# Optimization experiments

Measured on AMD Instinct MI355X. Metric: run time of the kernel, lower is better.

Reference implementation:

```python
import jax, jax.numpy as jnp
import numpy as np

N_HEADS = 16
N_KV_HEADS = 4
HEAD_DIM = 128
ROPE_THETA = 1000000.0

def setup_inputs() -> dict:
    key = jax.random.key(0)
    ks = jax.random.split(key, 5)
    B, T, D = 2, 2048, 2048
    s = 1.0 / np.sqrt(D)
    return {
        'x':  jax.random.normal(ks[0], (B, T, D), dtype=jnp.float32),
        'wq': jax.random.normal(ks[1], (D, N_HEADS * HEAD_DIM), dtype=jnp.float32) * s,
        'wk': jax.random.normal(ks[2], (D, N_KV_HEADS * HEAD_DIM), dtype=jnp.float32) * s,
        'wv': jax.random.normal(ks[3], (D, N_KV_HEADS * HEAD_DIM), dtype=jnp.float32) * s,
        'wo': jax.random.normal(ks[4], (N_HEADS * HEAD_DIM, D), dtype=jnp.float32) * s,
    }

def _rope_cos_sin(T, dtype):
    # build_rope_cache: inv_freq over half the head dim, cos/sin of shape [T, HEAD_DIM]
    half = HEAD_DIM // 2
    inv_freq = 1.0 / (ROPE_THETA ** (jnp.arange(0, half, dtype=jnp.float32) * 2.0 / HEAD_DIM))
    ang = jnp.arange(T, dtype=jnp.float32)[:, None] * inv_freq[None, :]  # [T, half]
    ang = jnp.concatenate([ang, ang], axis=-1)  # [T, HEAD_DIM]
    return jnp.cos(ang).astype(dtype), jnp.sin(ang).astype(dtype)

def _rotate_half(u):
    u1, u2 = jnp.split(u, 2, axis=-1)
    return jnp.concatenate([-u2, u1], axis=-1)

def _apply_rotary(h, cos, sin):
    # h: [B, H, T, hd]; cos/sin: [T, hd]
    return h * cos[None, None, :, :] + _rotate_half(h) * sin[None, None, :, :]

def _attention(x, wq, wk, wv, wo):
    B, T, D = x.shape
    dtype = x.dtype
    scale = HEAD_DIM ** -0.5
    # QKV projection + split heads -> [B, H, T, hd]
    qh = (x @ wq).reshape(B, T, N_HEADS, HEAD_DIM).transpose(0, 2, 1, 3)
    kh = (x @ wk).reshape(B, T, N_KV_HEADS, HEAD_DIM).transpose(0, 2, 1, 3)
    vh = (x @ wv).reshape(B, T, N_KV_HEADS, HEAD_DIM).transpose(0, 2, 1, 3)
    # RoPE
    cos, sin = _rope_cos_sin(T, dtype)
    qh = _apply_rotary(qh, cos, sin)
    kh = _apply_rotary(kh, cos, sin)
    # GQA: repeat kv heads
    rep = N_HEADS // N_KV_HEADS
    kh = jnp.repeat(kh, rep, axis=1)
    vh = jnp.repeat(vh, rep, axis=1)
    # eager attention: full score matrix [B, H, T, T]
    scores = jnp.einsum('bhtd,bhsd->bhts', qh, kh) * scale
    causal = jnp.tril(jnp.ones((T, T), dtype=bool))
    neg = jnp.asarray(jnp.finfo(jnp.float32).min, dtype=jnp.float32)
    scores = jnp.where(causal[None, None, :, :], scores.astype(jnp.float32), neg)
    probs = jax.nn.softmax(scores, axis=-1).astype(dtype)
    out = jnp.einsum('bhts,bhsd->bhtd', probs, vh)
    y = out.transpose(0, 2, 1, 3).reshape(B, T, N_HEADS * HEAD_DIM)  # merge heads
    return y @ wo

def reference(x, wq, wk, wv, wo):
    return _attention(x, wq, wk, wv, wo)
```

## Files before the change

### kernel.cpp

```cpp
#include <hip/hip_runtime.h>


#define T_SZ 2048
#define D_SZ 2048
#define BT   4096

typedef __attribute__((ext_vector_type(8))) short bf16x8;
typedef __attribute__((ext_vector_type(4))) float f32x4;

__device__ __forceinline__ unsigned short f2b(float f) {
  unsigned u = __float_as_uint(f);
  u = (u + 0x7fffu + ((u >> 16) & 1u)) >> 16;
  return (unsigned short)u;
}
__device__ __forceinline__ float b2f(unsigned short h) {
  return __uint_as_float(((unsigned)h) << 16);
}

__device__ __forceinline__ void async_ld16(const void* g, void* l) {
  __builtin_amdgcn_global_load_lds(
      (const __attribute__((address_space(1))) void*)g,
      (__attribute__((address_space(3))) void*)l, 16, 0, 0);
}

union Pack8 { unsigned short us[8]; uint4 v; };

__global__ __launch_bounds__(256) void cast_f32_bf16(
    const float* __restrict__ in, unsigned short* __restrict__ out) {
  int i = (blockIdx.x * 256 + threadIdx.x) * 4;
  float4 v = *(const float4*)(in + i);
  ushort4 o;
  o.x = f2b(v.x); o.y = f2b(v.y); o.z = f2b(v.z); o.w = f2b(v.w);
  *(ushort4*)(out + i) = o;
}

__global__ __launch_bounds__(256) void cast_transpose(
    const float* __restrict__ W, unsigned short* __restrict__ WT, int K, int N) {
  __shared__ float tile[64][68];
  int n0 = blockIdx.x * 64, k0 = blockIdx.y * 64;
  int t = threadIdx.x;
#pragma unroll
  for (int i = 0; i < 4; i++) {
    int c = t + 256 * i;
    int r = c >> 4, cc = c & 15;
    float4 v = *(const float4*)(W + (size_t)(k0 + r) * N + n0 + cc * 4);
    tile[r][cc * 4 + 0] = v.x; tile[r][cc * 4 + 1] = v.y;
    tile[r][cc * 4 + 2] = v.z; tile[r][cc * 4 + 3] = v.w;
  }
  __syncthreads();
#pragma unroll
  for (int i = 0; i < 2; i++) {
    int c = t + 256 * i;
    int n = c >> 3, kc = c & 7;
    Pack8 p;
#pragma unroll
    for (int j = 0; j < 8; j++) p.us[j] = f2b(tile[kc * 8 + j][n]);
    *(uint4*)(WT + (size_t)(n0 + n) * K + k0 + kc * 8) = p.v;
  }
}

template <int OUT_BF16>
__global__ __launch_bounds__(256) void gemm_bt(
    const unsigned short* __restrict__ A, const unsigned short* __restrict__ Bt,
    void* __restrict__ C, int M, int N, int K) {
  __shared__ unsigned short As[128 * 32];
  __shared__ unsigned short Bs[128 * 32];
  int t = threadIdx.x;
  int lane = t & 63, wave = t >> 6;
  int m0 = blockIdx.y * 128, n0 = blockIdx.x * 128;
  int wm = (wave >> 1) * 64, wn = (wave & 1) * 64;
  int fr = lane & 15, fq = lane >> 4;

  int srow = wave * 32 + (lane >> 2);
  int scol = (lane & 3) * 8;
  const unsigned short* Ag = A + (size_t)(m0 + srow) * K + scol;
  const unsigned short* Bg = Bt + (size_t)(n0 + srow) * K + scol;
  unsigned short* AsW = As + wave * 1024;
  unsigned short* BsW = Bs + wave * 1024;

  f32x4 acc[4][4];
#pragma unroll
  for (int mi = 0; mi < 4; mi++)
#pragma unroll
    for (int ni = 0; ni < 4; ni++) acc[mi][ni] = (f32x4){0.f, 0.f, 0.f, 0.f};

  for (int k0 = 0; k0 < K; k0 += 32) {
    __syncthreads();
#pragma unroll
    for (int j = 0; j < 2; j++) {
      async_ld16(Ag + (size_t)j * 16 * K + k0, AsW + j * 512);
      async_ld16(Bg + (size_t)j * 16 * K + k0, BsW + j * 512);
    }
    __syncthreads();
    bf16x8 a[4], b[4];
#pragma unroll
    for (int mi = 0; mi < 4; mi++)
      a[mi] = *(const bf16x8*)(As + (wm + 16 * mi + fr) * 32 + fq * 8);
#pragma unroll
    for (int ni = 0; ni < 4; ni++)
      b[ni] = *(const bf16x8*)(Bs + (wn + 16 * ni + fr) * 32 + fq * 8);
#pragma unroll
    for (int mi = 0; mi < 4; mi++)
#pragma unroll
      for (int ni = 0; ni < 4; ni++)
        acc[mi][ni] = __builtin_amdgcn_mfma_f32_16x16x32_bf16(
            a[mi], b[ni], acc[mi][ni], 0, 0, 0);
  }
#pragma unroll
  for (int mi = 0; mi < 4; mi++)
#pragma unroll
    for (int ni = 0; ni < 4; ni++)
#pragma unroll
      for (int r = 0; r < 4; r++) {
        int row = m0 + wm + 16 * mi + fq * 4 + r;
        int col = n0 + wn + 16 * ni + fr;
        float v = acc[mi][ni][r];
        if (OUT_BF16)
          ((unsigned short*)C)[(size_t)row * N + col] = f2b(v);
        else
          ((float*)C)[(size_t)row * N + col] = v;
      }
}

template <int LOGH, int STRIDE, int SCALE_Q>
__global__ __launch_bounds__(256) void rope_inplace(unsigned short* __restrict__ X) {
  int p = blockIdx.x * 256 + threadIdx.x;
  int d = p & 63;
  int h = (p >> 6) & ((1 << LOGH) - 1);
  int row = p >> (6 + LOGH);
  int tpos = row & (T_SZ - 1);
  size_t base = (size_t)row * STRIDE + h * 128 + d;
  float u1 = b2f(X[base]), u2 = b2f(X[base + 64]);
  float inv = expf(-(float)d * 0.21586735246819178f);
  float ang = (float)tpos * inv;
  float c = cosf(ang), s = sinf(ang);
  float o1 = u1 * c - u2 * s;
  float o2 = u2 * c + u1 * s;
  if (SCALE_Q) { o1 *= 0.08838834764831845f; o2 *= 0.08838834764831845f; }
  X[base]      = f2b(o1);
  X[base + 64] = f2b(o2);
}

__global__ __launch_bounds__(256) void transpose_v(
    const unsigned short* __restrict__ V ,
    unsigned short* __restrict__ VT) {
  __shared__ unsigned short tile[64][72];
  int t0 = blockIdx.x * 64;
  int n0 = blockIdx.y * 64;
  int bk = blockIdx.z;
  int b = bk >> 2, kvh = bk & 3;
  int t = threadIdx.x;
#pragma unroll
  for (int i = 0; i < 2; i++) {
    int c = t + 256 * i;
    int r = c >> 3, cc = c & 7;
    *(uint4*)&tile[r][cc * 8] = *(const uint4*)(
        V + (size_t)(b * T_SZ + t0 + r) * 3072 + kvh * 128 + n0 + cc * 8);
  }
  __syncthreads();
#pragma unroll
  for (int i = 0; i < 2; i++) {
    int c = t + 256 * i;
    int n = c >> 3, tc = c & 7;
    Pack8 p;
#pragma unroll
    for (int j = 0; j < 8; j++) p.us[j] = tile[tc * 8 + j][n];
    *(uint4*)(VT + ((size_t)bk * 128 + n0 + n) * T_SZ + t0 + tc * 8) = p.v;
  }
}

__global__ __launch_bounds__(512) void attn(
    const unsigned short* __restrict__ Q,
    const unsigned short* __restrict__ KV,
    const unsigned short* __restrict__ VT,
    unsigned short* __restrict__ O) {
  __shared__ unsigned short Ks[2][64 * 128];
  __shared__ unsigned short Vt[128 * 64];
  __shared__ unsigned short Ps[8][16 * 76];
  int qt = blockIdx.z ? blockIdx.x : 15 - blockIdx.x;
  int h = blockIdx.y, b = blockIdx.z;
  int kvh = h >> 2;
  int t = threadIdx.x, lane = t & 63, w = t >> 6;
  int fr = lane & 15, fq = lane >> 4;
  int rsw = fr & 7;

  bf16x8 qf[4];
#pragma unroll
  for (int kk = 0; kk < 4; kk++)
    qf[kk] = *(const bf16x8*)(
        Q + (size_t)(b * T_SZ + qt * 128 + w * 16 + fr) * 3072 +
        h * 128 + kk * 32 + fq * 8);

  const unsigned short* Kg = KV + (size_t)b * T_SZ * 3072 + kvh * 128;
  const unsigned short* Vg = VT + (size_t)(b * 4 + kvh) * 128 * T_SZ;

  int k_lr = lane >> 4, k_ls = lane & 15;
  int v_lr = lane >> 3, v_ls = lane & 7;

  auto stage_k = [&](int kt_, int bf) {
#pragma unroll
    for (int j = 0; j < 2; j++) {
      int row = w * 8 + j * 4 + k_lr;
      async_ld16(Kg + (size_t)(kt_ * 64 + row) * 3072 + ((k_ls ^ (row & 7)) << 3),
                 &Ks[bf][(w * 8 + j * 4) * 128]);
    }
  };
  auto stage_v = [&](int kt_) {
#pragma unroll
    for (int j = 0; j < 2; j++) {
      int row = w * 16 + j * 8 + v_lr;
      async_ld16(Vg + (size_t)row * T_SZ + kt_ * 64 + ((v_ls ^ (row & 7)) << 3),
                 &Vt[(w * 16 + j * 8) * 64]);
    }
  };

  f32x4 o[8];
#pragma unroll
  for (int i = 0; i < 8; i++) o[i] = (f32x4){0.f, 0.f, 0.f, 0.f};
  float mrow = -1e30f, lrow = 0.f;
  int qg = qt * 128 + w * 16 + fr;
  int nkt = 2 * qt + 2;

  stage_k(0, 0);
  stage_v(0);
  int cur = 0;
  for (int kt = 0; kt < nkt; kt++) {
    if (kt + 1 < nkt) {
      stage_k(kt + 1, cur ^ 1);
      asm volatile("s_waitcnt vmcnt(2)" ::: "memory");
    } else {
      asm volatile("s_waitcnt vmcnt(0)" ::: "memory");
    }
    __builtin_amdgcn_s_barrier();
    asm volatile("" ::: "memory");

    const unsigned short* KsC = Ks[cur];

    f32x4 s[4];
    __builtin_amdgcn_s_setprio(1);
#pragma unroll
    for (int nn = 0; nn < 4; nn++) {
      s[nn] = (f32x4){0.f, 0.f, 0.f, 0.f};
#pragma unroll
      for (int kk = 0; kk < 4; kk++) {
        bf16x8 kf = *(const bf16x8*)(
            KsC + (nn * 16 + fr) * 128 + ((((kk << 2) + fq) ^ rsw) << 3));
        s[nn] = __builtin_amdgcn_mfma_f32_16x16x32_bf16(kf, qf[kk], s[nn], 0, 0, 0);
      }
    }
    __builtin_amdgcn_s_setprio(0);
    if (kt * 64 + 63 > qg) {
#pragma unroll
      for (int nn = 0; nn < 4; nn++)
#pragma unroll
        for (int r = 0; r < 4; r++) {
          int kvg = kt * 64 + nn * 16 + fq * 4 + r;
          if (kvg > qg) s[nn][r] = -1e30f;
        }
    }
    f32x4 t4;
#pragma unroll
    for (int r = 0; r < 4; r++)
      t4[r] = fmaxf(fmaxf(s[0][r], s[1][r]), fmaxf(s[2][r], s[3][r]));
    float mx = fmaxf(fmaxf(t4[0], t4[1]), fmaxf(t4[2], t4[3]));
    mx = fmaxf(mx, __shfl_xor(mx, 16, 64));
    mx = fmaxf(mx, __shfl_xor(mx, 32, 64));
    float mnew = fmaxf(mrow, mx);
    float sum = 0.f;
#pragma unroll
    for (int nn = 0; nn < 4; nn++) {
      ushort4 pk;
      float p0 = __expf(s[nn][0] - mnew); pk.x = f2b(p0);
      float p1 = __expf(s[nn][1] - mnew); pk.y = f2b(p1);
      float p2 = __expf(s[nn][2] - mnew); pk.z = f2b(p2);
      float p3 = __expf(s[nn][3] - mnew); pk.w = f2b(p3);
      sum += (p0 + p1) + (p2 + p3);
      *(ushort4*)(Ps[w] + fr * 76 + nn * 16 + fq * 4) = pk;
    }
    float alpha = __expf(mrow - mnew);
    lrow = lrow * alpha + sum;
    mrow = mnew;
#pragma unroll
    for (int nt = 0; nt < 8; nt++)
#pragma unroll
      for (int r = 0; r < 4; r++) o[nt][r] *= alpha;
    __builtin_amdgcn_s_setprio(1);
#pragma unroll
    for (int kk = 0; kk < 2; kk++) {
      bf16x8 pf = *(const bf16x8*)(Ps[w] + fr * 76 + kk * 32 + fq * 8);
#pragma unroll
      for (int nt = 0; nt < 8; nt++) {
        bf16x8 vf = *(const bf16x8*)(
            Vt + (nt * 16 + fr) * 64 + ((((kk << 2) + fq) ^ rsw) << 3));
        o[nt] = __builtin_amdgcn_mfma_f32_16x16x32_bf16(vf, pf, o[nt], 0, 0, 0);
      }
    }
    __builtin_amdgcn_s_setprio(0);
    asm volatile("s_waitcnt lgkmcnt(0)" ::: "memory");
    __builtin_amdgcn_s_barrier();
    asm volatile("" ::: "memory");
    if (kt + 1 < nkt) stage_v(kt + 1);
    cur ^= 1;
  }
  float lsum = lrow;
  lsum += __shfl_xor(lsum, 16, 64);
  lsum += __shfl_xor(lsum, 32, 64);
  float linv = 1.f / lsum;
  int rowg = b * T_SZ + qt * 128 + w * 16 + fr;
#pragma unroll
  for (int nt = 0; nt < 8; nt++) {
    ushort4 ov;
    ov.x = f2b(o[nt][0] * linv);
    ov.y = f2b(o[nt][1] * linv);
    ov.z = f2b(o[nt][2] * linv);
    ov.w = f2b(o[nt][3] * linv);
    *(ushort4*)(O + (size_t)rowg * 2048 + h * 128 + nt * 16 + fq * 4) = ov;
  }
}

extern "C" void kernel_launch(void* const* d_in, const int* in_sizes, int n_in,
                              void* d_out, int out_size, void* d_ws, size_t ws_size,
                              hipStream_t stream) {
  const float* x  = (const float*)d_in[0];
  const float* wq = (const float*)d_in[1];
  const float* wk = (const float*)d_in[2];
  const float* wv = (const float*)d_in[3];
  const float* wo = (const float*)d_in[4];
  float* out = (float*)d_out;

  unsigned short* xb   = (unsigned short*)d_ws;
  unsigned short* wqT  = xb   + (size_t)4096 * 2048;
  unsigned short* wkT  = wqT  + (size_t)2048 * 2048;
  unsigned short* wvT  = wkT  + (size_t)512 * 2048;
  unsigned short* woT  = wvT  + (size_t)512 * 2048;
  unsigned short* QKVb = woT  + (size_t)2048 * 2048;
  unsigned short* VTb  = QKVb + (size_t)4096 * 3072;
  unsigned short* AOb  = VTb  + (size_t)4096 * 512;

  cast_f32_bf16<<<8192, 256, 0, stream>>>(x, xb);
  cast_transpose<<<dim3(32, 32), 256, 0, stream>>>(wq, wqT, 2048, 2048);
  cast_transpose<<<dim3(8, 32),  256, 0, stream>>>(wk, wkT, 2048, 512);
  cast_transpose<<<dim3(8, 32),  256, 0, stream>>>(wv, wvT, 2048, 512);
  cast_transpose<<<dim3(32, 32), 256, 0, stream>>>(wo, woT, 2048, 2048);

  gemm_bt<1><<<dim3(24, 32), 256, 0, stream>>>(xb, wqT, QKVb, 4096, 3072, 2048);

  rope_inplace<4, 3072, 1><<<16384, 256, 0, stream>>>(QKVb);
  rope_inplace<2, 3072, 0><<<4096,  256, 0, stream>>>(QKVb + 2048);
  transpose_v<<<dim3(32, 2, 8), 256, 0, stream>>>(QKVb + 2560, VTb);

  attn<<<dim3(16, 16, 2), 512, 0, stream>>>(QKVb, QKVb + 2048, VTb, AOb);

  gemm_bt<0><<<dim3(16, 32), 256, 0, stream>>>(AOb, woT, (void*)out, 4096, 2048, 2048);
}
```

Measured before the change: 334.0 us.

## Fuse Q RoPE into attention, double-buffer V, and alias P onto K tile

Drops the separate RoPE pass over Q. Each attention wave now rotates and pre-scales its Q fragments in registers with sincosf and expf after issuing the first K/V loads, which removes one full read-modify-write of Q in global memory and one kernel launch. V is now double-buffered like K, and its next tile is issued right after the top barrier, replacing the end-of-iteration lgkmcnt wait and barrier. The softmax P tile moves out of its own LDS array into each wave's own slice of the current K buffer, using a swizzled layout, after a new barrier that follows QK^T. This keeps LDS usage about the same while adding a V buffer, at the cost of per-block transcendental math and a mid-iteration barrier.

```diff
diff --git a/kernel.cpp b/kernel.cpp
--- a/kernel.cpp
+++ b/kernel.cpp
@@ -175,8 +175,7 @@
     const unsigned short* __restrict__ VT,
     unsigned short* __restrict__ O) {
   __shared__ unsigned short Ks[2][64 * 128];
-  __shared__ unsigned short Vt[128 * 64];
-  __shared__ unsigned short Ps[8][16 * 76];
+  __shared__ unsigned short Vt[2][128 * 64];
   int qt = blockIdx.z ? blockIdx.x : 15 - blockIdx.x;
   int h = blockIdx.y, b = blockIdx.z;
   int kvh = h >> 2;
@@ -205,14 +204,34 @@
                  &Ks[bf][(w * 8 + j * 4) * 128]);
     }
   };
-  auto stage_v = [&](int kt_) {
+  auto stage_v = [&](int kt_, int bf) {
 #pragma unroll
     for (int j = 0; j < 2; j++) {
       int row = w * 16 + j * 8 + v_lr;
       async_ld16(Vg + (size_t)row * T_SZ + kt_ * 64 + ((v_ls ^ (row & 7)) << 3),
-                 &Vt[(w * 16 + j * 8) * 64]);
+                 &Vt[bf][(w * 16 + j * 8) * 64]);
     }
   };
+
+  stage_k(0, 0);
+  stage_v(0, 0);
+
+  {
+    float tposf = (float)(qt * 128 + w * 16 + fr);
+#pragma unroll
+    for (int kk = 0; kk < 2; kk++)
+#pragma unroll
+      for (int j = 0; j < 8; j++) {
+        int d = kk * 32 + (fq << 3) + j;
+        float u1 = b2f((unsigned short)qf[kk][j]);
+        float u2 = b2f((unsigned short)qf[kk + 2][j]);
+        float inv = expf(-(float)d * 0.21586735246819178f);
+        float ang = tposf * inv, c, s;
+        sincosf(ang, &s, &c);
+        qf[kk][j]     = (short)f2b((u1 * c - u2 * s) * 0.08838834764831845f);
+        qf[kk + 2][j] = (short)f2b((u2 * c + u1 * s) * 0.08838834764831845f);
+      }
+  }
 
   f32x4 o[8];
 #pragma unroll
@@ -221,8 +240,6 @@
   int qg = qt * 128 + w * 16 + fr;
   int nkt = 2 * qt + 2;
 
-  stage_k(0, 0);
-  stage_v(0);
   int cur = 0;
   for (int kt = 0; kt < nkt; kt++) {
     if (kt + 1 < nkt) {
@@ -233,8 +250,11 @@
     }
     __builtin_amdgcn_s_barrier();
     asm volatile("" ::: "memory");
+    if (kt + 1 < nkt) stage_v(kt + 1, cur ^ 1);
 
     const unsigned short* KsC = Ks[cur];
+    const unsigned short* VtC = Vt[cur];
+    unsigned short* PsW = (unsigned short*)&Ks[cur][w * 1024];
 
     f32x4 s[4];
     __builtin_amdgcn_s_setprio(1);
@@ -249,6 +269,9 @@
       }
     }
     __builtin_amdgcn_s_setprio(0);
+    __builtin_amdgcn_s_barrier();
+    asm volatile("" ::: "memory");
+
     if (kt * 64 + 63 > qg) {
 #pragma unroll
       for (int nn = 0; nn < 4; nn++)
@@ -275,7 +298,8 @@
       float p2 = __expf(s[nn][2] - mnew); pk.z = f2b(p2);
       float p3 = __expf(s[nn][3] - mnew); pk.w = f2b(p3);
       sum += (p0 + p1) + (p2 + p3);
-      *(ushort4*)(Ps[w] + fr * 76 + nn * 16 + fq * 4) = pk;
+      int pslot = ((nn * 2 + (fq >> 1)) ^ rsw);
+      *(ushort4*)(PsW + fr * 64 + (pslot << 3) + ((fq & 1) << 2)) = pk;
     }
     float alpha = __expf(mrow - mnew);
     lrow = lrow * alpha + sum;
@@ -287,19 +311,16 @@
     __builtin_amdgcn_s_setprio(1);
 #pragma unroll
     for (int kk = 0; kk < 2; kk++) {
-      bf16x8 pf = *(const bf16x8*)(Ps[w] + fr * 76 + kk * 32 + fq * 8);
+      bf16x8 pf = *(const bf16x8*)(
+          PsW + fr * 64 + ((((kk << 2) + fq) ^ rsw) << 3));
 #pragma unroll
       for (int nt = 0; nt < 8; nt++) {
         bf16x8 vf = *(const bf16x8*)(
-            Vt + (nt * 16 + fr) * 64 + ((((kk << 2) + fq) ^ rsw) << 3));
+            VtC + (nt * 16 + fr) * 64 + ((((kk << 2) + fq) ^ rsw) << 3));
         o[nt] = __builtin_amdgcn_mfma_f32_16x16x32_bf16(vf, pf, o[nt], 0, 0, 0);
       }
     }
     __builtin_amdgcn_s_setprio(0);
-    asm volatile("s_waitcnt lgkmcnt(0)" ::: "memory");
-    __builtin_amdgcn_s_barrier();
-    asm volatile("" ::: "memory");
-    if (kt + 1 < nkt) stage_v(kt + 1);
     cur ^= 1;
   }
   float lsum = lrow;
@@ -345,8 +366,7 @@
 
   gemm_bt<1><<<dim3(24, 32), 256, 0, stream>>>(xb, wqT, QKVb, 4096, 3072, 2048);
 
-  rope_inplace<4, 3072, 1><<<16384, 256, 0, stream>>>(QKVb);
-  rope_inplace<2, 3072, 0><<<4096,  256, 0, stream>>>(QKVb + 2048);
+  rope_inplace<2, 3072, 0><<<4096, 256, 0, stream>>>(QKVb + 2048);
   transpose_v<<<dim3(32, 2, 8), 256, 0, stream>>>(QKVb + 2560, VTb);
 
   attn<<<dim3(16, 16, 2), 512, 0, stream>>>(QKVb, QKVb + 2048, VTb, AOb);
```

New measurement: 370.4 us. +10.9%, slower.
